# Optimization experiments

Measured on AMD Instinct MI355X. Metric: run time of the kernel, lower is better.

The kernel has to match this reference:

```python
import jax, jax.numpy as jnp
import numpy as np
import math

B, S, H, A = 16, 2048, 1024, 64
SCALE = math.sqrt(A)

def setup_inputs() -> dict:
    key = jax.random.key(0)
    ks = jax.random.split(key, 8)
    x = jax.random.normal(ks[0], (B, S, H), dtype=jnp.float32)
    mask = jax.random.randint(ks[1], (B, S), 0, 2).astype(jnp.int32)
    Wq = jax.random.normal(ks[2], (H, A), dtype=jnp.float32) / math.sqrt(H)
    bq = jnp.zeros((A,), dtype=jnp.float32)
    Wk = jax.random.normal(ks[3], (H, A), dtype=jnp.float32) / math.sqrt(H)
    bk = jnp.zeros((A,), dtype=jnp.float32)
    Wv = jax.random.normal(ks[4], (H, H), dtype=jnp.float32) / math.sqrt(H)
    bv = jnp.zeros((H,), dtype=jnp.float32)
    return {"x": x, "mask": mask, "Wq": Wq, "bq": bq, "Wk": Wk, "bk": bk, "Wv": Wv, "bv": bv}

def reference(x, mask, Wq, bq, Wk, bk, Wv, bv):
    # x: (B,S,H), mask: (B,S) int {0,1}
    Q = x @ Wq + bq            # (B,S,A)
    K = x @ Wk + bk            # (B,S,A)
    V = x @ Wv + bv            # (B,S,H)
    scores = jnp.einsum('bsa,bta->bst', Q, K) / SCALE  # (B,S,S)
    scores = jnp.where(mask[:, None, :] == 0, -jnp.inf, scores)
    attn = jax.nn.softmax(scores, axis=-1)
    attn = jnp.nan_to_num(attn, nan=0.0)  # rows fully masked -> 0
    context = jnp.einsum('bst,bth->bsh', attn, V)      # (B,S,H)
    m = mask[:, :, None].astype(context.dtype)          # (B,S,1)
    context = context * m
    output = context.sum(axis=1) / (m.sum(axis=1) + 1e-8)  # (B,H)
    return output, attn.mean(axis=1)                    # (B,H), (B,S)
```

## Files before the change

kernel.cpp:

```cpp
#include <hip/hip_runtime.h>
#include <math.h>

#define BN_ 16
#define SS  2048
#define HH  1024

typedef unsigned short u16;
typedef unsigned int   u32;
typedef __bf16 bf16x8 __attribute__((ext_vector_type(8)));
typedef float  f32x4  __attribute__((ext_vector_type(4)));
typedef float  f32x16 __attribute__((ext_vector_type(16)));
#define MFMA16 __builtin_amdgcn_mfma_f32_16x16x32_bf16
#define MFMA32 __builtin_amdgcn_mfma_f32_32x32x16_bf16

#define QK_OFF    0
#define QK_FLOATS (BN_*SS*64)
#define WT_OFF    (QK_OFF + QK_FLOATS)
#define WT_FLOATS (64*HH)
#define CP_OFF    (WT_OFF + WT_FLOATS)
#define CP_FLOATS (BN_*32*2*SS)
#define NB_OFF    (CP_OFF + CP_FLOATS)
#define NBW_OFF   (NB_OFF + 16)
#define U_OFF     (NBW_OFF + 16)

__device__ __forceinline__ u16 f2b(float f) {
    unsigned u = __builtin_bit_cast(unsigned, f);
    return (u16)((u + 0x7FFFu + ((u >> 16) & 1u)) >> 16);
}

__device__ __forceinline__ bf16x8 cvt8(float4 a, float4 b) {
    bf16x8 r;
    r[0] = (__bf16)a.x; r[1] = (__bf16)a.y; r[2] = (__bf16)a.z; r[3] = (__bf16)a.w;
    r[4] = (__bf16)b.x; r[5] = (__bf16)b.y; r[6] = (__bf16)b.z; r[7] = (__bf16)b.w;
    return r;
}

__device__ __forceinline__ int swze(int row, int e) {
    return row * 64 + (e ^ ((row & 7) << 3));
}

__device__ __forceinline__ bf16x8 ldfrag(const u16* t, int row16, int ks, int l6) {
    int row = row16 + (l6 & 15);
    int e = ks * 32 + ((l6 >> 4) << 3);
    return *(const bf16x8*)&t[swze(row, e)];
}

__device__ __forceinline__ void gload16(const u16* g, u16* l) {
    __builtin_amdgcn_global_load_lds(
        (const __attribute__((address_space(1))) u32*)g,
        (__attribute__((address_space(3))) u32*)l, 16, 0, 0);
}

__global__ __launch_bounds__(256) void k_prep(const float* __restrict__ Wq,
                                              const float* __restrict__ Wk,
                                              const int* __restrict__ mask,
                                              u16* __restrict__ wt,
                                              float* __restrict__ nbv,
                                              float* __restrict__ nbw,
                                              float* __restrict__ u,
                                              float* __restrict__ outz) {
    int bid = blockIdx.x, tid = threadIdx.x;
    if (bid < 128) {
        const float* src = (bid < 64) ? &Wq[bid] : &Wk[bid - 64];
        for (int k = tid; k < HH; k += 256)
            wt[(size_t)bid * HH + k] = f2b(src[(size_t)k * 64]);
    } else if (bid < 144) {
        int b = bid - 128;
        int s = 0;
        for (int i = tid; i < SS; i += 256) s += mask[b * SS + i];
        float fs = (float)s;
        for (int off = 1; off < 64; off <<= 1) fs += __shfl_xor(fs, off);
        __shared__ float red[4];
        if ((tid & 63) == 0) red[tid >> 6] = fs;
        __syncthreads();
        if (tid == 0) {
            float t = red[0] + red[1] + red[2] + red[3];
            nbv[b] = t + 1e-8f;
            nbw[b] = t / (t + 1e-8f);
        }
    } else {
        int zb = bid - 144;
        float* dst = (zb < 8) ? (u + zb * 2048) : (outz + (zb - 8) * 2048);
        for (int i = tid; i < 2048; i += 256) dst[i] = 0.f;
    }
}

__global__ __launch_bounds__(256) void k_qkproj(const float* __restrict__ x,
                                                const u16* __restrict__ wt,
                                                const float* __restrict__ bq,
                                                const float* __restrict__ bk,
                                                u16* __restrict__ qk) {
    __shared__ __align__(16) u16 Bs[4][128 * 64];
    int tid = threadIdx.x, l6 = tid & 63, w = tid >> 6;
    int lr = l6 & 15, lk = l6 >> 4;
    int row = blockIdx.x * 64 + w * 16;
    const float* xr = x + (size_t)(row + lr) * HH + lk * 8;
    int r0 = tid >> 3, j = tid & 7;
    const u16* bsrc = wt + (size_t)r0 * HH + (j ^ (r0 & 7)) * 8;
    float4 xa0[4], xa1[4];
    #define GLOADB(kt, BI) { const u16* s_ = bsrc + (kt) * 64; u16* l_ = Bs[BI] + tid * 8;  \
        gload16(s_,            l_);        gload16(s_ + 32 * HH, l_ + 2048);                \
        gload16(s_ + 64 * HH,  l_ + 4096); gload16(s_ + 96 * HH, l_ + 6144); }
    #define LOADA(kt, A_) { const float* p_ = xr + (kt) * 64;                               \
        A_[0] = *(const float4*)p_;        A_[1] = *(const float4*)(p_ + 4);                \
        A_[2] = *(const float4*)(p_ + 32); A_[3] = *(const float4*)(p_ + 36); }
    #define COMP(BI, A_) { const u16* Bp = Bs[BI];                                          \
        bf16x8 a0 = cvt8(A_[0], A_[1]);                                                     \
        bf16x8 a1 = cvt8(A_[2], A_[3]);                                                     \
        _Pragma("unroll")                                                                   \
        for (int jj = 0; jj < 8; ++jj) {                                                    \
            bf16x8 b0 = ldfrag(Bp, jj * 16, 0, l6);                                         \
            bf16x8 b1 = ldfrag(Bp, jj * 16, 1, l6);                                         \
            acc[jj] = MFMA16(a0, b0, acc[jj], 0, 0, 0);                                     \
            acc[jj] = MFMA16(a1, b1, acc[jj], 0, 0, 0);                                     \
        } }

    f32x4 acc[8];
    #pragma unroll
    for (int jj = 0; jj < 8; ++jj) acc[jj] = (f32x4){0.f, 0.f, 0.f, 0.f};

    GLOADB(0, 0); GLOADB(1, 1); LOADA(0, xa0); LOADA(1, xa1);
    __syncthreads();
    for (int p = 0; p < 8; ++p) {
        int k0 = 2 * p;
        if (p < 7) { GLOADB(k0 + 2, (k0 + 2) & 3); GLOADB(k0 + 3, (k0 + 3) & 3); }
        __builtin_amdgcn_s_setprio(1);
        COMP(k0 & 3, xa0);
        __builtin_amdgcn_s_setprio(0);
        if (p < 7) LOADA(k0 + 2, xa0);
        __builtin_amdgcn_s_setprio(1);
        COMP((k0 + 1) & 3, xa1);
        __builtin_amdgcn_s_setprio(0);
        if (p < 7) {
            LOADA(k0 + 3, xa1);
            __syncthreads();
        }
    }
    #pragma unroll
    for (int jj = 0; jj < 8; ++jj) {
        int n = jj * 16 + lr;
        float bias = (n < 64) ? bq[n] : bk[n - 64];
        int mrow = row + lk * 4;
        #pragma unroll
        for (int r4 = 0; r4 < 4; ++r4)
            qk[(size_t)(mrow + r4) * 128 + n] = f2b(acc[jj][r4] + bias);
    }
    #undef GLOADB
    #undef LOADA
    #undef COMP
}

__global__ __launch_bounds__(256) void k_score(const u16* __restrict__ qk,
                                               const int* __restrict__ mask,
                                               float* __restrict__ cpart) {
    __shared__ __align__(16) u16 Ks0[128 * 64];
    __shared__ __align__(16) u16 Ks1[128 * 64];
    __shared__ float pml[SS];
    __shared__ float redbuf[4][64];
    __shared__ float lshs[64];
    int l = blockIdx.x;
    int b = (l & 7) * 2 + ((l >> 3) >> 5);
    int sb = (l >> 3) & 31;
    int tid = threadIdx.x, l6 = tid & 63, w = tid >> 6;
    int cl = l6 & 31, hi = l6 >> 5;
    for (int i = tid; i < SS; i += 256) pml[i] = mask[b * SS + i] ? 0.f : -1e30f;
    const u16* qkb = qk + (size_t)b * SS * 128;
    int q0 = sb * 64;
    bf16x8 qA[2][4];
    #pragma unroll
    for (int rs = 0; rs < 2; ++rs)
        #pragma unroll
        for (int ks = 0; ks < 4; ++ks)
            qA[rs][ks] = *(const bf16x8*)&qkb[(size_t)(q0 + rs * 32 + cl) * 128 + ks * 16 + hi * 8];
    int r0 = tid >> 3, j = tid & 7;
    const u16* ksrc = qkb + 64 + (size_t)r0 * 128 + (j ^ (r0 & 7)) * 8;
    #define GLOADK(tt, B_) { const u16* s_ = ksrc + (size_t)(tt) * (128 * 128); u16* l_ = B_ + tid * 8; \
        gload16(s_,             l_);        gload16(s_ + 32 * 128, l_ + 2048);                          \
        gload16(s_ + 64 * 128,  l_ + 4096); gload16(s_ + 96 * 128, l_ + 6144); }

    const float SCL = 0.18033688f;
    GLOADK(0, Ks0);
    __syncthreads();
    float rsum[2][16];
    #pragma unroll
    for (int rs = 0; rs < 2; ++rs)
        #pragma unroll
        for (int r = 0; r < 16; ++r) rsum[rs][r] = 0.f;
    for (int tt = 0; tt < 16; ++tt) {
        const u16* Ks = (tt & 1) ? Ks1 : Ks0;
        if (tt < 15) {
            if (tt & 1) { GLOADK(tt + 1, Ks0); } else { GLOADK(tt + 1, Ks1); }
        }
        bf16x8 kB[4];
        #pragma unroll
        for (int ks = 0; ks < 4; ++ks)
            kB[ks] = *(const bf16x8*)&Ks[swze(w * 32 + cl, ks * 16 + hi * 8)];
        float pmv = pml[tt * 128 + w * 32 + cl];
        __builtin_amdgcn_s_setprio(1);
        #pragma unroll
        for (int rs = 0; rs < 2; ++rs) {
            f32x16 acc = {};
            #pragma unroll
            for (int ks = 0; ks < 4; ++ks) acc = MFMA32(qA[rs][ks], kB[ks], acc, 0, 0, 0);
            #pragma unroll
            for (int r = 0; r < 16; ++r)
                rsum[rs][r] += exp2f(fmaf(acc[r], SCL, pmv));
        }
        __builtin_amdgcn_s_setprio(0);
        if (tt < 15) __syncthreads();
    }
    #pragma unroll
    for (int off = 1; off < 32; off <<= 1)
        #pragma unroll
        for (int rs = 0; rs < 2; ++rs)
            #pragma unroll
            for (int r = 0; r < 16; ++r)
                rsum[rs][r] += __shfl_xor(rsum[rs][r], off);
    if (cl == 0) {
        #pragma unroll
        for (int rs = 0; rs < 2; ++rs)
            #pragma unroll
            for (int r = 0; r < 16; ++r)
                redbuf[w][rs * 32 + (r & 3) + 8 * (r >> 2) + 4 * hi] = rsum[rs][r];
    }
    GLOADK(0, Ks0);
    __syncthreads();
    if (tid < 64) {
        float lv = redbuf[0][tid] + redbuf[1][tid] + redbuf[2][tid] + redbuf[3][tid];
        lshs[tid] = (lv > 0.f) ? -log2f(lv) : -1e30f;
    }
    __syncthreads();
    float lsh[2][16];
    unsigned qmb = 0;
    #pragma unroll
    for (int rs = 0; rs < 2; ++rs)
        #pragma unroll
        for (int r = 0; r < 16; ++r) {
            int rowi = rs * 32 + (r & 3) + 8 * (r >> 2) + 4 * hi;
            lsh[rs][r] = lshs[rowi];
            qmb |= (pml[q0 + rowi] == 0.f ? 1u : 0u) << (rs * 16 + r);
        }
    for (int tt = 0; tt < 16; ++tt) {
        const u16* Ks = (tt & 1) ? Ks1 : Ks0;
        if (tt < 15) {
            if (tt & 1) { GLOADK(tt + 1, Ks0); } else { GLOADK(tt + 1, Ks1); }
        }
        bf16x8 kB[4];
        #pragma unroll
        for (int ks = 0; ks < 4; ++ks)
            kB[ks] = *(const bf16x8*)&Ks[swze(w * 32 + cl, ks * 16 + hi * 8)];
        float pmv = pml[tt * 128 + w * 32 + cl];
        float sa = 0.f, sm = 0.f;
        __builtin_amdgcn_s_setprio(1);
        #pragma unroll
        for (int rs = 0; rs < 2; ++rs) {
            f32x16 acc = {};
            #pragma unroll
            for (int ks = 0; ks < 4; ++ks) acc = MFMA32(qA[rs][ks], kB[ks], acc, 0, 0, 0);
            #pragma unroll
            for (int r = 0; r < 16; ++r) {
                float e = exp2f(fmaf(acc[r], SCL, lsh[rs][r]) + pmv);
                sa += e;
                sm += ((qmb >> (rs * 16 + r)) & 1u) ? e : 0.f;
            }
        }
        __builtin_amdgcn_s_setprio(0);
        sa += __shfl_xor(sa, 32);
        sm += __shfl_xor(sm, 32);
        if (hi == 0) {
            size_t base = (((size_t)b * 32 + sb) * 2) * SS + tt * 128 + w * 32 + cl;
            cpart[base] = sa;
            cpart[base + SS] = sm;
        }
        if (tt < 15) __syncthreads();
    }
    #undef GLOADK
}

__global__ __launch_bounds__(256) void k_u(const float* __restrict__ x,
                                           const float* __restrict__ cpart,
                                           const int* __restrict__ mask,
                                           const float* __restrict__ nbv,
                                           float* __restrict__ u,
                                           float* __restrict__ out_mean) {
    __shared__ float wl[64];
    __shared__ float red2[2][4][64];
    int b = blockIdx.x, ch = blockIdx.y;
    int tid = threadIdx.x, tl = tid & 63, qd = tid >> 6;
    int t = ch * 64 + tl;
    float sa = 0.f, sm = 0.f;
    #pragma unroll
    for (int k = 0; k < 8; ++k) {
        const float* p = &cpart[(((size_t)b * 32 + (qd * 8 + k)) * 2) * SS + t];
        sa += p[0];
        sm += p[SS];
    }
    red2[0][qd][tl] = sa;
    red2[1][qd][tl] = sm;
    __syncthreads();
    if (tid < 64) {
        float sat = red2[0][0][tl] + red2[0][1][tl] + red2[0][2][tl] + red2[0][3][tl];
        float smt = red2[1][0][tl] + red2[1][1][tl] + red2[1][2][tl] + red2[1][3][tl];
        float pm = mask[b * SS + t] ? 1.f : 0.f;
        out_mean[b * SS + t] = sat * pm * (1.f / SS);
        wl[tl] = smt * pm / nbv[b];
    }
    __syncthreads();
    const float* xb = &x[((size_t)b * SS + ch * 64) * HH + tid * 4];
    float4 acc = {0.f, 0.f, 0.f, 0.f};
    #pragma unroll 16
    for (int tt = 0; tt < 64; ++tt) {
        float4 xv = *(const float4*)&xb[(size_t)tt * HH];
        float wv = wl[tt];
        acc.x += wv * xv.x; acc.y += wv * xv.y;
        acc.z += wv * xv.z; acc.w += wv * xv.w;
    }
    float* up = &u[(size_t)b * HH + tid * 4];
    atomicAdd(&up[0], acc.x);
    atomicAdd(&up[1], acc.y);
    atomicAdd(&up[2], acc.z);
    atomicAdd(&up[3], acc.w);
}

__global__ __launch_bounds__(256) void k_out0a(const float* __restrict__ u,
                                               const float* __restrict__ Wv,
                                               const float* __restrict__ bv,
                                               const float* __restrict__ nbw,
                                               float* __restrict__ out) {
    __shared__ float uT[64][16];
    __shared__ float red[4][64][16];
    int cb = blockIdx.x, hb = blockIdx.y;
    int c0 = cb * 64, h0 = hb * 64;
    int tid = threadIdx.x;
    int hl = tid & 63, cq = tid >> 6;
    #pragma unroll
    for (int it = 0; it < 4; ++it) {
        int b = it * 4 + cq;
        uT[hl][b] = u[(size_t)b * HH + c0 + hl];
    }
    __syncthreads();
    int h = h0 + hl;
    float acc[16];
    #pragma unroll
    for (int b = 0; b < 16; ++b) acc[b] = 0.f;
    #pragma unroll
    for (int cc = 0; cc < 16; ++cc) {
        int c = cq * 16 + cc;
        float wv = Wv[(size_t)(c0 + c) * HH + h];
        #pragma unroll
        for (int b = 0; b < 16; ++b) acc[b] += uT[c][b] * wv;
    }
    #pragma unroll
    for (int b = 0; b < 16; ++b) red[cq][hl][b] = acc[b];
    __syncthreads();
    #pragma unroll
    for (int it = 0; it < 4; ++it) {
        int b = it * 4 + cq;
        float s = red[0][hl][b] + red[1][hl][b] + red[2][hl][b] + red[3][hl][b];
        if (cb == 0) s += bv[h] * nbw[b];
        atomicAdd(&out[(size_t)b * HH + h], s);
    }
}

extern "C" void kernel_launch(void* const* d_in, const int* in_sizes, int n_in,
                              void* d_out, int out_size, void* d_ws, size_t ws_size,
                              hipStream_t stream) {
    const float* x  = (const float*)d_in[0];
    const int* mask = (const int*)d_in[1];
    const float* Wq = (const float*)d_in[2];
    const float* bq = (const float*)d_in[3];
    const float* Wk = (const float*)d_in[4];
    const float* bk = (const float*)d_in[5];
    const float* Wv = (const float*)d_in[6];
    const float* bv = (const float*)d_in[7];
    float* out = (float*)d_out;
    float* ws  = (float*)d_ws;

    u16*   qk    = (u16*)(ws + QK_OFF);
    u16*   wt    = (u16*)(ws + WT_OFF);
    float* cpart = ws + CP_OFF;
    float* nbv   = ws + NB_OFF;
    float* nbw   = ws + NBW_OFF;
    float* u     = ws + U_OFF;

    k_prep   <<<dim3(160),        dim3(256), 0, stream>>>(Wq, Wk, mask, wt, nbv, nbw, u, out);
    k_qkproj <<<dim3(512),        dim3(256), 0, stream>>>(x, wt, bq, bk, qk);
    k_score  <<<dim3(512),        dim3(256), 0, stream>>>(qk, mask, cpart);
    k_u      <<<dim3(BN_, 32),    dim3(256), 0, stream>>>(x, cpart, mask, nbv, u, out + BN_ * HH);
    k_out0a  <<<dim3(16, 16),     dim3(256), 0, stream>>>(u, Wv, bv, nbw, out);
}
```

Baseline: 127.4 us.

## Quad-buffer K tiles in score kernel and coalesce weight transpose in prep

The score kernel moves from double-buffered K tiles with one barrier per tile to four LDS buffers, loading two tiles ahead and syncing once per pair of tiles. The aim is to halve barrier count and give the async global-to-LDS loads more time to complete. The prep kernel's Wq/Wk transpose now reads coalesced rows across 64 blocks instead of strided column reads across 128 blocks. The extra LDS (64KB for K plus the mask buffer) may lower occupancy.

```diff
diff --git a/kernel.cpp b/kernel.cpp
--- a/kernel.cpp
+++ b/kernel.cpp
@@ -60,12 +60,16 @@
                                               float* __restrict__ u,
                                               float* __restrict__ outz) {
     int bid = blockIdx.x, tid = threadIdx.x;
-    if (bid < 128) {
-        const float* src = (bid < 64) ? &Wq[bid] : &Wk[bid - 64];
-        for (int k = tid; k < HH; k += 256)
-            wt[(size_t)bid * HH + k] = f2b(src[(size_t)k * 64]);
-    } else if (bid < 144) {
-        int b = bid - 128;
+    if (bid < 64) {
+        int i4 = tid >> 6, n = tid & 63;
+        #pragma unroll
+        for (int ii = 0; ii < 4; ++ii) {
+            int k = bid * 16 + ii * 4 + i4;
+            wt[(size_t)n * HH + k]        = f2b(Wq[(size_t)k * 64 + n]);
+            wt[(size_t)(64 + n) * HH + k] = f2b(Wk[(size_t)k * 64 + n]);
+        }
+    } else if (bid < 80) {
+        int b = bid - 64;
         int s = 0;
         for (int i = tid; i < SS; i += 256) s += mask[b * SS + i];
         float fs = (float)s;
@@ -79,7 +83,7 @@
             nbw[b] = t / (t + 1e-8f);
         }
     } else {
-        int zb = bid - 144;
+        int zb = bid - 80;
         float* dst = (zb < 8) ? (u + zb * 2048) : (outz + (zb - 8) * 2048);
         for (int i = tid; i < 2048; i += 256) dst[i] = 0.f;
     }
@@ -153,8 +157,7 @@
 __global__ __launch_bounds__(256) void k_score(const u16* __restrict__ qk,
                                                const int* __restrict__ mask,
                                                float* __restrict__ cpart) {
-    __shared__ __align__(16) u16 Ks0[128 * 64];
-    __shared__ __align__(16) u16 Ks1[128 * 64];
+    __shared__ __align__(16) u16 Ks[4 * 8192];
     __shared__ float pml[SS];
     __shared__ float redbuf[4][64];
     __shared__ float lshs[64];
@@ -174,40 +177,44 @@
             qA[rs][ks] = *(const bf16x8*)&qkb[(size_t)(q0 + rs * 32 + cl) * 128 + ks * 16 + hi * 8];
     int r0 = tid >> 3, j = tid & 7;
     const u16* ksrc = qkb + 64 + (size_t)r0 * 128 + (j ^ (r0 & 7)) * 8;
-    #define GLOADK(tt, B_) { const u16* s_ = ksrc + (size_t)(tt) * (128 * 128); u16* l_ = B_ + tid * 8; \
-        gload16(s_,             l_);        gload16(s_ + 32 * 128, l_ + 2048);                          \
+    #define GLOADK(tt, BI) { const u16* s_ = ksrc + (size_t)(tt) * (128 * 128);             \
+        u16* l_ = Ks + (BI) * 8192 + tid * 8;                                               \
+        gload16(s_,             l_);        gload16(s_ + 32 * 128, l_ + 2048);              \
         gload16(s_ + 64 * 128,  l_ + 4096); gload16(s_ + 96 * 128, l_ + 6144); }
 
     const float SCL = 0.18033688f;
-    GLOADK(0, Ks0);
-    __syncthreads();
     float rsum[2][16];
     #pragma unroll
     for (int rs = 0; rs < 2; ++rs)
         #pragma unroll
         for (int r = 0; r < 16; ++r) rsum[rs][r] = 0.f;
-    for (int tt = 0; tt < 16; ++tt) {
-        const u16* Ks = (tt & 1) ? Ks1 : Ks0;
-        if (tt < 15) {
-            if (tt & 1) { GLOADK(tt + 1, Ks0); } else { GLOADK(tt + 1, Ks1); }
-        }
-        bf16x8 kB[4];
-        #pragma unroll
-        for (int ks = 0; ks < 4; ++ks)
-            kB[ks] = *(const bf16x8*)&Ks[swze(w * 32 + cl, ks * 16 + hi * 8)];
-        float pmv = pml[tt * 128 + w * 32 + cl];
-        __builtin_amdgcn_s_setprio(1);
-        #pragma unroll
-        for (int rs = 0; rs < 2; ++rs) {
-            f32x16 acc = {};
-            #pragma unroll
-            for (int ks = 0; ks < 4; ++ks) acc = MFMA32(qA[rs][ks], kB[ks], acc, 0, 0, 0);
-            #pragma unroll
-            for (int r = 0; r < 16; ++r)
-                rsum[rs][r] += exp2f(fmaf(acc[r], SCL, pmv));
-        }
-        __builtin_amdgcn_s_setprio(0);
-        if (tt < 15) __syncthreads();
+
+    #define P1C(tt, BI) { const u16* KsB = Ks + (BI) * 8192;                                \
+        bf16x8 kB[4];                                                                       \
+        _Pragma("unroll")                                                                   \
+        for (int ks = 0; ks < 4; ++ks)                                                      \
+            kB[ks] = *(const bf16x8*)&KsB[swze(w * 32 + cl, ks * 16 + hi * 8)];             \
+        float pmv = pml[(tt) * 128 + w * 32 + cl];                                          \
+        __builtin_amdgcn_s_setprio(1);                                                      \
+        _Pragma("unroll")                                                                   \
+        for (int rs = 0; rs < 2; ++rs) {                                                    \
+            f32x16 a_ = {};                                                                 \
+            _Pragma("unroll")                                                               \
+            for (int ks = 0; ks < 4; ++ks) a_ = MFMA32(qA[rs][ks], kB[ks], a_, 0, 0, 0);    \
+            _Pragma("unroll")                                                               \
+            for (int r = 0; r < 16; ++r)                                                    \
+                rsum[rs][r] += exp2f(fmaf(a_[r], SCL, pmv));                                \
+        }                                                                                   \
+        __builtin_amdgcn_s_setprio(0); }
+
+    GLOADK(0, 0); GLOADK(1, 1);
+    __syncthreads();
+    for (int p = 0; p < 8; ++p) {
+        int t0 = 2 * p;
+        if (p < 7) { GLOADK(t0 + 2, (t0 + 2) & 3); GLOADK(t0 + 3, (t0 + 3) & 3); }
+        P1C(t0, t0 & 3);
+        P1C(t0 + 1, (t0 + 1) & 3);
+        if (p < 7) __syncthreads();
     }
     #pragma unroll
     for (int off = 1; off < 32; off <<= 1)
@@ -223,7 +230,7 @@
             for (int r = 0; r < 16; ++r)
                 redbuf[w][rs * 32 + (r & 3) + 8 * (r >> 2) + 4 * hi] = rsum[rs][r];
     }
-    GLOADK(0, Ks0);
+    GLOADK(0, 0); GLOADK(1, 1);
     __syncthreads();
     if (tid < 64) {
         float lv = redbuf[0][tid] + redbuf[1][tid] + redbuf[2][tid] + redbuf[3][tid];
@@ -240,41 +247,44 @@
             lsh[rs][r] = lshs[rowi];
             qmb |= (pml[q0 + rowi] == 0.f ? 1u : 0u) << (rs * 16 + r);
         }
-    for (int tt = 0; tt < 16; ++tt) {
-        const u16* Ks = (tt & 1) ? Ks1 : Ks0;
-        if (tt < 15) {
-            if (tt & 1) { GLOADK(tt + 1, Ks0); } else { GLOADK(tt + 1, Ks1); }
-        }
-        bf16x8 kB[4];
-        #pragma unroll
-        for (int ks = 0; ks < 4; ++ks)
-            kB[ks] = *(const bf16x8*)&Ks[swze(w * 32 + cl, ks * 16 + hi * 8)];
-        float pmv = pml[tt * 128 + w * 32 + cl];
-        float sa = 0.f, sm = 0.f;
-        __builtin_amdgcn_s_setprio(1);
-        #pragma unroll
-        for (int rs = 0; rs < 2; ++rs) {
-            f32x16 acc = {};
-            #pragma unroll
-            for (int ks = 0; ks < 4; ++ks) acc = MFMA32(qA[rs][ks], kB[ks], acc, 0, 0, 0);
-            #pragma unroll
-            for (int r = 0; r < 16; ++r) {
-                float e = exp2f(fmaf(acc[r], SCL, lsh[rs][r]) + pmv);
-                sa += e;
-                sm += ((qmb >> (rs * 16 + r)) & 1u) ? e : 0.f;
-            }
-        }
-        __builtin_amdgcn_s_setprio(0);
-        sa += __shfl_xor(sa, 32);
-        sm += __shfl_xor(sm, 32);
-        if (hi == 0) {
-            size_t base = (((size_t)b * 32 + sb) * 2) * SS + tt * 128 + w * 32 + cl;
-            cpart[base] = sa;
-            cpart[base + SS] = sm;
-        }
-        if (tt < 15) __syncthreads();
+
+    #define P2C(tt, BI) { const u16* KsB = Ks + (BI) * 8192;                                \
+        bf16x8 kB[4];                                                                       \
+        _Pragma("unroll")                                                                   \
+        for (int ks = 0; ks < 4; ++ks)                                                      \
+            kB[ks] = *(const bf16x8*)&KsB[swze(w * 32 + cl, ks * 16 + hi * 8)];             \
+        float pmv = pml[(tt) * 128 + w * 32 + cl];                                          \
+        float sa = 0.f, sm = 0.f;                                                           \
+        __builtin_amdgcn_s_setprio(1);                                                      \
+        _Pragma("unroll")                                                                   \
+        for (int rs = 0; rs < 2; ++rs) {                                                    \
+            f32x16 a_ = {};                                                                 \
+            _Pragma("unroll")                                                               \
+            for (int ks = 0; ks < 4; ++ks) a_ = MFMA32(qA[rs][ks], kB[ks], a_, 0, 0, 0);    \
+            _Pragma("unroll")                                                               \
+            for (int r = 0; r < 16; ++r) {                                                  \
+                float e_ = exp2f(fmaf(a_[r], SCL, lsh[rs][r]) + pmv);                       \
+                sa += e_;                                                                   \
+                sm += ((qmb >> (rs * 16 + r)) & 1u) ? e_ : 0.f;                             \
+            }                                                                               \
+        }                                                                                   \
+        __builtin_amdgcn_s_setprio(0);                                                      \
+        sa += __shfl_xor(sa, 32); sm += __shfl_xor(sm, 32);                                 \
+        if (hi == 0) {                                                                      \
+            size_t b_ = (((size_t)b * 32 + sb) * 2) * SS + (size_t)(tt) * 128 + w * 32 + cl; \
+            cpart[b_] = sa; cpart[b_ + SS] = sm;                                            \
+        } }
+
+    for (int p = 0; p < 8; ++p) {
+        int t0 = 2 * p;
+        if (p < 7) { GLOADK(t0 + 2, (t0 + 2) & 3); GLOADK(t0 + 3, (t0 + 3) & 3); }
+        P2C(t0, t0 & 3);
+        P2C(t0 + 1, (t0 + 1) & 3);
+        if (p < 7) __syncthreads();
     }
     #undef GLOADK
+    #undef P1C
+    #undef P2C
 }
 
 __global__ __launch_bounds__(256) void k_u(const float* __restrict__ x,
@@ -383,7 +393,7 @@
     float* nbw   = ws + NBW_OFF;
     float* u     = ws + U_OFF;
 
-    k_prep   <<<dim3(160),        dim3(256), 0, stream>>>(Wq, Wk, mask, wt, nbv, nbw, u, out);
+    k_prep   <<<dim3(96),         dim3(256), 0, stream>>>(Wq, Wk, mask, wt, nbv, nbw, u, out);
     k_qkproj <<<dim3(512),        dim3(256), 0, stream>>>(x, wt, bq, bk, qk);
     k_score  <<<dim3(512),        dim3(256), 0, stream>>>(qk, mask, cpart);
     k_u      <<<dim3(BN_, 32),    dim3(256), 0, stream>>>(x, cpart, mask, nbv, u, out + BN_ * HH);
```

Result: no change. 127.8 us (+0.3%).
